# Optimization experiments

Measured on AMD Instinct MI355X. Metric: run time of the kernel, lower is better.

Reference implementation:

```python
import jax, jax.numpy as jnp
import numpy as np

NUM_SEGMENTS = 4096  # number of graphs in the batch


def setup_inputs() -> dict:
    key = jax.random.key(0)
    k1, k2, k3, k4, k5, k6 = jax.random.split(key, 6)
    N, H = 1048576, 128
    x = jax.random.normal(k1, (N, H), dtype=jnp.float32)
    batch = jnp.sort(jax.random.randint(k2, (N,), 0, NUM_SEGMENTS, dtype=jnp.int64))
    # Linear params, PyTorch layout: W [out, in], b [out]
    W1 = jax.random.normal(k3, (2 * H, H), dtype=jnp.float32) * (1.0 / np.sqrt(H))
    b1 = jax.random.normal(k4, (2 * H,), dtype=jnp.float32) * 0.01
    W2 = jax.random.normal(k5, (H, 2 * H), dtype=jnp.float32) * (1.0 / np.sqrt(2 * H))
    b2 = jax.random.normal(k6, (H,), dtype=jnp.float32) * 0.01
    return {"x": x, "batch": batch, "W1": W1, "b1": b1, "W2": W2, "b2": b2}


def reference(x, batch, W1, b1, W2, b2):
    # phi(x) = tanh(fc1(x))  -> [N, 2H]
    phi_x = jnp.tanh(jnp.einsum('nh,oh->no', x, W1) + b1)
    # scatter-sum pooling per graph -> [G, 2H]
    sum_x = jax.ops.segment_sum(phi_x, batch, num_segments=NUM_SEGMENTS)
    # fc2 -> [G, H]; .squeeze() is a no-op for these shapes
    y = jnp.einsum('go,ho->gh', sum_x, W2) + b2
    return jnp.squeeze(y)
```

## Files before the change

kernel.cpp:

```cpp
#include <hip/hip_runtime.h>
#include <hip/hip_bf16.h>

#define NTOT 1048576
#define NSEG 4096
#define HDIM 128
#define ODIM 256
#define BN   64
#define GRID1 1024
#define TPB  (NTOT / (BN * GRID1))

typedef __attribute__((ext_vector_type(8))) short bf16x8;
typedef __attribute__((ext_vector_type(4))) float f32x4;
typedef __attribute__((ext_vector_type(4))) unsigned int u32x4;

typedef const __attribute__((address_space(1))) unsigned int* gp_t;
typedef __attribute__((address_space(3))) unsigned int* lp_t;

__device__ __forceinline__ unsigned int cvt_pk(float lo, float hi) {
    unsigned int r;
    asm("v_cvt_pk_bf16_f32 %0, %1, %2" : "=v"(r) : "v"(lo), "v"(hi));
    return r;
}

__global__ void zero_convert(const float* __restrict__ W1, unsigned int* __restrict__ W1b,
                             float* __restrict__ sumx) {
    int gid = blockIdx.x * 256 + threadIdx.x;
    sumx[gid] = 0.0f;
    if (gid < (ODIM * HDIM / 2)) {
        float2 v = *(const float2*)(W1 + 2 * gid);
        W1b[gid] = cvt_pk(v.x, v.y);
    }
}

__global__ __launch_bounds__(256, 2)
void stage1(const float* __restrict__ x, const int* __restrict__ batch,
            const unsigned short* __restrict__ W1b, const float* __restrict__ b1,
            float* __restrict__ sumx) {
    __shared__ __align__(16) float xbuf[2][BN * HDIM];
    __shared__ int segAll[TPB * BN];

    const int t    = threadIdx.x;
    const int lane = t & 63;
    const int wv   = t >> 6;
    const int l15  = lane & 15;
    const int lhi  = (lane >> 4) & 3;

    const bool is64 = (batch[NTOT - 1] == 0);
    const long r0 = (long)blockIdx.x * (TPB * BN);
    const char* xb = (const char*)(x + r0 * HDIM);

    int doff[8];
    #pragma unroll
    for (int j = 0; j < 8; ++j) {
        int b   = wv * 8 + j;
        int row = ((b >> 1) & 3) * 16 + l15;
        int c4  = (b >> 3) * 8 + lhi * 2 + (b & 1);
        doff[j] = row * 512 + c4 * 16;
    }

    #pragma unroll
    for (int j = 0; j < 8; ++j)
        __builtin_amdgcn_global_load_lds((gp_t)(xb + doff[j]),
                                         (lp_t)(&xbuf[0][(wv * 8 + j) * 64 * 4]), 16, 0, 0);
    __builtin_amdgcn_sched_barrier(0);

    for (int i = t; i < TPB * BN; i += 256) {
        long idx = r0 + i;
        segAll[i] = batch[is64 ? 2 * idx : idx];
    }
    bf16x8 bfr[4][4];
    #pragma unroll
    for (int nf = 0; nf < 4; ++nf)
        #pragma unroll
        for (int ks = 0; ks < 4; ++ks)
            bfr[nf][ks] = *(const bf16x8*)(W1b + (wv * 64 + nf * 16 + l15) * HDIM + ks * 32 + lhi * 8);
    float bias[4];
    #pragma unroll
    for (int nf = 0; nf < 4; ++nf) bias[nf] = b1[wv * 64 + nf * 16 + l15];

    asm volatile("s_waitcnt vmcnt(0) lgkmcnt(0)" ::: "memory");
    __builtin_amdgcn_sched_barrier(0);
    __builtin_amdgcn_s_barrier();

    for (int g = 0; g < TPB; ++g) {
        const int nb = g & 1;

        if (g + 1 < TPB) {
            const char* src = xb + (size_t)(g + 1) * (BN * HDIM * 4);
            #pragma unroll
            for (int j = 0; j < 8; ++j)
                __builtin_amdgcn_global_load_lds((gp_t)(src + doff[j]),
                                                 (lp_t)(&xbuf[nb ^ 1][(wv * 8 + j) * 64 * 4]), 16, 0, 0);
            __builtin_amdgcn_sched_barrier(0);
            asm volatile("s_waitcnt vmcnt(8)" ::: "memory");
        } else {
            asm volatile("s_waitcnt vmcnt(0)" ::: "memory");
        }
        __builtin_amdgcn_sched_barrier(0);
        __builtin_amdgcn_s_barrier();
        __builtin_amdgcn_sched_barrier(0);

        f32x4 acc[4][4];
        #pragma unroll
        for (int nf = 0; nf < 4; ++nf) {
            const float bb = bias[nf];
            #pragma unroll
            for (int mf = 0; mf < 4; ++mf)
                acc[mf][nf] = (f32x4){bb, bb, bb, bb};
        }
        const f32x4* fb = (const f32x4*)&xbuf[nb][0];
        #pragma unroll
        for (int ks = 0; ks < 4; ++ks) {
            #pragma unroll
            for (int mf = 0; mf < 4; ++mf) {
                f32x4 u = fb[(ks * 8 + mf * 2) * 64 + lane];
                f32x4 v = fb[(ks * 8 + mf * 2 + 1) * 64 + lane];
                u32x4 w;
                w.x = cvt_pk(u.x, u.y); w.y = cvt_pk(u.z, u.w);
                w.z = cvt_pk(v.x, v.y); w.w = cvt_pk(v.z, v.w);
                bf16x8 af = __builtin_bit_cast(bf16x8, w);
                #pragma unroll
                for (int nf = 0; nf < 4; ++nf)
                    acc[mf][nf] = __builtin_amdgcn_mfma_f32_16x16x32_bf16(af, bfr[nf][ks], acc[mf][nf], 0, 0, 0);
            }
        }

        #pragma unroll
        for (int mf = 0; mf < 4; ++mf)
            #pragma unroll
            for (int nf = 0; nf < 4; ++nf)
                #pragma unroll
                for (int r = 0; r < 4; ++r) {
                    float e = exp2f(acc[mf][nf][r] * 2.885390081777927f);
                    acc[mf][nf][r] = 1.0f - 2.0f * __builtin_amdgcn_rcpf(1.0f + e);
                }

        const int* segc = &segAll[g * BN];
        unsigned long long bmask;
        {
            int s_here = segc[lane];
            int s_prev = (lane > 0) ? segc[lane - 1] : s_here;
            bmask = __ballot(s_here != s_prev);
        }
        int start = 0;
        unsigned long long rem = bmask;
        for (;;) {
            const int end = rem ? (int)__builtin_ctzll(rem) : BN;
            const int sid = segc[start];
            float p0 = 0.f, p1 = 0.f, p2 = 0.f, p3 = 0.f;
            #pragma unroll
            for (int mf = 0; mf < 4; ++mf)
                #pragma unroll
                for (int r = 0; r < 4; ++r) {
                    int row = mf * 16 + lhi * 4 + r;
                    float w = ((unsigned)(row - start) < (unsigned)(end - start)) ? 1.0f : 0.0f;
                    p0 = fmaf(w, acc[mf][0][r], p0);
                    p1 = fmaf(w, acc[mf][1][r], p1);
                    p2 = fmaf(w, acc[mf][2][r], p2);
                    p3 = fmaf(w, acc[mf][3][r], p3);
                }
            p0 += __shfl_xor(p0, 16); p0 += __shfl_xor(p0, 32);
            p1 += __shfl_xor(p1, 16); p1 += __shfl_xor(p1, 32);
            p2 += __shfl_xor(p2, 16); p2 += __shfl_xor(p2, 32);
            p3 += __shfl_xor(p3, 16); p3 += __shfl_xor(p3, 32);
            if (lhi == 0) {
                float* base = sumx + (long)sid * ODIM + wv * 64 + l15;
                atomicAdd(base +  0, p0);
                atomicAdd(base + 16, p1);
                atomicAdd(base + 32, p2);
                atomicAdd(base + 48, p3);
            }
            if (rem == 0) break;
            start = end;
            rem &= rem - 1;
        }

        asm volatile("s_waitcnt lgkmcnt(0)" ::: "memory");
        __builtin_amdgcn_sched_barrier(0);
        __builtin_amdgcn_s_barrier();
        __builtin_amdgcn_sched_barrier(0);
    }
}

__global__ __launch_bounds__(256)
void stage2(const float* __restrict__ sumx, const float* __restrict__ W2,
            const float* __restrict__ b2, float* __restrict__ y) {
    __shared__ float sx[16 * 256];
    const int t = threadIdx.x;
    const long g0 = (long)blockIdx.x * 16;
    #pragma unroll
    for (int i = 0; i < 16; ++i)
        sx[i * 256 + t] = sumx[(g0 + i) * 256 + t];
    __syncthreads();
    const int h = t & 127;
    const int gl0 = (t >> 7) * 8;
    float acc[8] = {0, 0, 0, 0, 0, 0, 0, 0};
    const float* w = W2 + h * 256;
    for (int o4 = 0; o4 < 64; ++o4) {
        float4 wvv = *(const float4*)(w + o4 * 4);
        #pragma unroll
        for (int gl = 0; gl < 8; ++gl) {
            const float* sr = &sx[(gl0 + gl) * 256 + o4 * 4];
            acc[gl] += sr[0] * wvv.x + sr[1] * wvv.y + sr[2] * wvv.z + sr[3] * wvv.w;
        }
    }
    float bb = b2[h];
    #pragma unroll
    for (int gl = 0; gl < 8; ++gl)
        y[(g0 + gl0 + gl) * 128 + h] = acc[gl] + bb;
}

extern "C" void kernel_launch(void* const* d_in, const int* in_sizes, int n_in,
                              void* d_out, int out_size, void* d_ws, size_t ws_size,
                              hipStream_t stream) {
    const float* x   = (const float*)d_in[0];
    const int* batch = (const int*)d_in[1];
    const float* W1  = (const float*)d_in[2];
    const float* b1  = (const float*)d_in[3];
    const float* W2  = (const float*)d_in[4];
    const float* b2  = (const float*)d_in[5];
    float* y = (float*)d_out;

    float* sumx = (float*)d_ws;
    unsigned short* W1b = (unsigned short*)((char*)d_ws + (size_t)NSEG * ODIM * 4);

    zero_convert<<<dim3(NSEG), dim3(256), 0, stream>>>(W1, (unsigned int*)W1b, sumx);
    stage1<<<dim3(GRID1), dim3(256), 0, stream>>>(x, batch, W1b, b1, sumx);
    stage2<<<dim3(NSEG / 16), dim3(256), 0, stream>>>(sumx, W2, b2, y);
}
```

Measured before the change: 217.9 us.

## Deepen x prefetch to 4-stage ring and split output columns across 8 waves

New measurement: 288.4 us. +32.3%, slower.

```diff
diff --git a/kernel.cpp b/kernel.cpp
--- a/kernel.cpp
+++ b/kernel.cpp
@@ -6,8 +6,9 @@
 #define HDIM 128
 #define ODIM 256
 #define BN   64
-#define GRID1 1024
+#define GRID1 256
 #define TPB  (NTOT / (BN * GRID1))
+#define NBUF 4
 
 typedef __attribute__((ext_vector_type(8))) short bf16x8;
 typedef __attribute__((ext_vector_type(4))) float f32x4;
@@ -32,11 +33,11 @@
     }
 }
 
-__global__ __launch_bounds__(256, 2)
+__global__ __launch_bounds__(512, 2)
 void stage1(const float* __restrict__ x, const int* __restrict__ batch,
             const unsigned short* __restrict__ W1b, const float* __restrict__ b1,
             float* __restrict__ sumx) {
-    __shared__ __align__(16) float xbuf[2][BN * HDIM];
+    __shared__ __align__(16) float xbuf[NBUF][BN * HDIM];
     __shared__ int segAll[TPB * BN];
 
     const int t    = threadIdx.x;
@@ -49,66 +50,70 @@
     const long r0 = (long)blockIdx.x * (TPB * BN);
     const char* xb = (const char*)(x + r0 * HDIM);
 
-    int doff[8];
-    #pragma unroll
-    for (int j = 0; j < 8; ++j) {
-        int b   = wv * 8 + j;
+    int doff[4];
+    #pragma unroll
+    for (int j = 0; j < 4; ++j) {
+        int b   = wv * 4 + j;
         int row = ((b >> 1) & 3) * 16 + l15;
         int c4  = (b >> 3) * 8 + lhi * 2 + (b & 1);
         doff[j] = row * 512 + c4 * 16;
     }
 
     #pragma unroll
-    for (int j = 0; j < 8; ++j)
-        __builtin_amdgcn_global_load_lds((gp_t)(xb + doff[j]),
-                                         (lp_t)(&xbuf[0][(wv * 8 + j) * 64 * 4]), 16, 0, 0);
+    for (int tt = 0; tt < 3; ++tt) {
+        const char* src = xb + (size_t)tt * (BN * HDIM * 4);
+        #pragma unroll
+        for (int j = 0; j < 4; ++j)
+            __builtin_amdgcn_global_load_lds((gp_t)(src + doff[j]),
+                                             (lp_t)(&xbuf[tt][(wv * 4 + j) * 256]), 16, 0, 0);
+    }
     __builtin_amdgcn_sched_barrier(0);
 
-    for (int i = t; i < TPB * BN; i += 256) {
+    for (int i = t; i < TPB * BN; i += 512) {
         long idx = r0 + i;
         segAll[i] = batch[is64 ? 2 * idx : idx];
     }
-    bf16x8 bfr[4][4];
-    #pragma unroll
-    for (int nf = 0; nf < 4; ++nf)
+    bf16x8 bfr[2][4];
+    #pragma unroll
+    for (int nf = 0; nf < 2; ++nf)
         #pragma unroll
         for (int ks = 0; ks < 4; ++ks)
-            bfr[nf][ks] = *(const bf16x8*)(W1b + (wv * 64 + nf * 16 + l15) * HDIM + ks * 32 + lhi * 8);
-    float bias[4];
-    #pragma unroll
-    for (int nf = 0; nf < 4; ++nf) bias[nf] = b1[wv * 64 + nf * 16 + l15];
-
-    asm volatile("s_waitcnt vmcnt(0) lgkmcnt(0)" ::: "memory");
+            bfr[nf][ks] = *(const bf16x8*)(W1b + (wv * 32 + nf * 16 + l15) * HDIM + ks * 32 + lhi * 8);
+    float bias[2];
+    #pragma unroll
+    for (int nf = 0; nf < 2; ++nf) bias[nf] = b1[wv * 32 + nf * 16 + l15];
+
+    asm volatile("s_waitcnt lgkmcnt(0)" ::: "memory");
     __builtin_amdgcn_sched_barrier(0);
     __builtin_amdgcn_s_barrier();
 
     for (int g = 0; g < TPB; ++g) {
-        const int nb = g & 1;
-
-        if (g + 1 < TPB) {
-            const char* src = xb + (size_t)(g + 1) * (BN * HDIM * 4);
-            #pragma unroll
-            for (int j = 0; j < 8; ++j)
+        if (g + 3 < TPB) {
+            const char* src = xb + (size_t)(g + 3) * (BN * HDIM * 4);
+            float* dst = &xbuf[(g + 3) & (NBUF - 1)][0];
+            #pragma unroll
+            for (int j = 0; j < 4; ++j)
                 __builtin_amdgcn_global_load_lds((gp_t)(src + doff[j]),
-                                                 (lp_t)(&xbuf[nb ^ 1][(wv * 8 + j) * 64 * 4]), 16, 0, 0);
+                                                 (lp_t)(dst + (wv * 4 + j) * 256), 16, 0, 0);
             __builtin_amdgcn_sched_barrier(0);
-            asm volatile("s_waitcnt vmcnt(8)" ::: "memory");
-        } else {
-            asm volatile("s_waitcnt vmcnt(0)" ::: "memory");
-        }
+        }
+        if (g < TPB - 3)       asm volatile("s_waitcnt vmcnt(12)" ::: "memory");
+        else if (g == TPB - 3) asm volatile("s_waitcnt vmcnt(8)"  ::: "memory");
+        else if (g == TPB - 2) asm volatile("s_waitcnt vmcnt(4)"  ::: "memory");
+        else                   asm volatile("s_waitcnt vmcnt(0)"  ::: "memory");
         __builtin_amdgcn_sched_barrier(0);
         __builtin_amdgcn_s_barrier();
         __builtin_amdgcn_sched_barrier(0);
 
-        f32x4 acc[4][4];
-        #pragma unroll
-        for (int nf = 0; nf < 4; ++nf) {
+        f32x4 acc[4][2];
+        #pragma unroll
+        for (int nf = 0; nf < 2; ++nf) {
             const float bb = bias[nf];
             #pragma unroll
             for (int mf = 0; mf < 4; ++mf)
                 acc[mf][nf] = (f32x4){bb, bb, bb, bb};
         }
-        const f32x4* fb = (const f32x4*)&xbuf[nb][0];
+        const f32x4* fb = (const f32x4*)&xbuf[g & (NBUF - 1)][0];
         #pragma unroll
         for (int ks = 0; ks < 4; ++ks) {
             #pragma unroll
@@ -120,7 +125,7 @@
                 w.z = cvt_pk(v.x, v.y); w.w = cvt_pk(v.z, v.w);
                 bf16x8 af = __builtin_bit_cast(bf16x8, w);
                 #pragma unroll
-                for (int nf = 0; nf < 4; ++nf)
+                for (int nf = 0; nf < 2; ++nf)
                     acc[mf][nf] = __builtin_amdgcn_mfma_f32_16x16x32_bf16(af, bfr[nf][ks], acc[mf][nf], 0, 0, 0);
             }
         }
@@ -128,7 +133,7 @@
         #pragma unroll
         for (int mf = 0; mf < 4; ++mf)
             #pragma unroll
-            for (int nf = 0; nf < 4; ++nf)
+            for (int nf = 0; nf < 2; ++nf)
                 #pragma unroll
                 for (int r = 0; r < 4; ++r) {
                     float e = exp2f(acc[mf][nf][r] * 2.885390081777927f);
@@ -147,7 +152,7 @@
         for (;;) {
             const int end = rem ? (int)__builtin_ctzll(rem) : BN;
             const int sid = segc[start];
-            float p0 = 0.f, p1 = 0.f, p2 = 0.f, p3 = 0.f;
+            float p0 = 0.f, p1 = 0.f;
             #pragma unroll
             for (int mf = 0; mf < 4; ++mf)
                 #pragma unroll
@@ -156,19 +161,13 @@
                     float w = ((unsigned)(row - start) < (unsigned)(end - start)) ? 1.0f : 0.0f;
                     p0 = fmaf(w, acc[mf][0][r], p0);
                     p1 = fmaf(w, acc[mf][1][r], p1);
-                    p2 = fmaf(w, acc[mf][2][r], p2);
-                    p3 = fmaf(w, acc[mf][3][r], p3);
                 }
             p0 += __shfl_xor(p0, 16); p0 += __shfl_xor(p0, 32);
             p1 += __shfl_xor(p1, 16); p1 += __shfl_xor(p1, 32);
-            p2 += __shfl_xor(p2, 16); p2 += __shfl_xor(p2, 32);
-            p3 += __shfl_xor(p3, 16); p3 += __shfl_xor(p3, 32);
             if (lhi == 0) {
-                float* base = sumx + (long)sid * ODIM + wv * 64 + l15;
+                float* base = sumx + (long)sid * ODIM + wv * 32 + l15;
                 atomicAdd(base +  0, p0);
                 atomicAdd(base + 16, p1);
-                atomicAdd(base + 32, p2);
-                atomicAdd(base + 48, p3);
             }
             if (rem == 0) break;
             start = end;
@@ -225,6 +224,6 @@
     unsigned short* W1b = (unsigned short*)((char*)d_ws + (size_t)NSEG * ODIM * 4);
 
     zero_convert<<<dim3(NSEG), dim3(256), 0, stream>>>(W1, (unsigned int*)W1b, sumx);
-    stage1<<<dim3(GRID1), dim3(256), 0, stream>>>(x, batch, W1b, b1, sumx);
+    stage1<<<dim3(GRID1), dim3(512), 0, stream>>>(x, batch, W1b, b1, sumx);
     stage2<<<dim3(NSEG / 16), dim3(256), 0, stream>>>(sumx, W2, b2, y);
 }
```
